# Kernel tuning notes

Hardware: AMD Instinct MI355X
Metric: run time of the kernel (lower is better)

## Reference

```python
import jax, jax.numpy as jnp
import numpy as np
import math

D_KEY = 64
D_VALUE = 64
NUM_HEADS = 16
D_MODEL = D_VALUE * NUM_HEADS  # 1024


def setup_inputs() -> dict:
    key = jax.random.key(0)
    ks = jax.random.split(key, 5)
    B, N = 2, 2048
    s = 1.0 / math.sqrt(D_MODEL)
    return {
        "x": jax.random.normal(ks[0], (B, N, D_MODEL), dtype=jnp.float32),
        "Wq": jax.random.normal(ks[1], (D_MODEL, D_KEY * NUM_HEADS), dtype=jnp.float32) * s,
        "Wk": jax.random.normal(ks[2], (D_MODEL, D_KEY * NUM_HEADS), dtype=jnp.float32) * s,
        "Wv": jax.random.normal(ks[3], (D_MODEL, D_MODEL), dtype=jnp.float32) * s,
        "Wp": jax.random.normal(ks[4], (D_MODEL, D_MODEL), dtype=jnp.float32) * s,
    }


def reference(x, Wq, Wk, Wv, Wp):
    # x: [B, N, d_model]. Equivalent to the original block-diagonal concat trick:
    # off-diagonal blocks are -inf, so softmax over the key axis reduces to
    # independent per-head softmax attention.
    B, N, D = x.shape
    H, K, V = NUM_HEADS, D_KEY, D_VALUE
    scale = 1.0 / math.sqrt(K)
    q = (x @ Wq).reshape(B, N, H, K)
    k = (x @ Wk).reshape(B, N, H, K)
    v = (x @ Wv).reshape(B, N, H, V)
    scores = jnp.einsum("bnhk,bmhk->bhnm", q, k) * scale  # [B,H,N,N]
    attn = jax.nn.softmax(scores, axis=-1)
    out = jnp.einsum("bhnm,bmhv->bnhv", attn, v).reshape(B, N, D)
    return x + out @ Wp
```

## Files before the change

kernel.cpp:

```cpp
#include <hip/hip_runtime.h>

typedef float f32x4 __attribute__((ext_vector_type(4)));
typedef __bf16 bf16x8 __attribute__((ext_vector_type(8)));

#define DEV static __device__ __forceinline__

DEV ushort f2bf(float f) {
  unsigned u = __builtin_bit_cast(unsigned, f);
  u += 0x7FFFu + ((u >> 16) & 1u);
  return (ushort)(u >> 16);
}

DEV bf16x8 ld_frag(const ushort* p) {
  return __builtin_bit_cast(bf16x8, *reinterpret_cast<const int4*>(p));
}

DEV bf16x8 ld_lds(const ushort* base, int byte_off) {
  return __builtin_bit_cast(bf16x8,
      *reinterpret_cast<const int4*>(reinterpret_cast<const char*>(base) + byte_off));
}

DEV int swz(int row, int col_byte) { return row * 128 + (col_byte ^ ((row & 7) << 4)); }

DEV float fast_exp2(float x) {
  float r;
  asm("v_exp_f32 %0, %1" : "=v"(r) : "v"(x));
  return r;
}

DEV unsigned cvt_pk_bf16(float lo, float hi) {
  unsigned r;
  asm("v_cvt_pk_bf16_f32 %0, %1, %2" : "=v"(r) : "v"(lo), "v"(hi));
  return r;
}

DEV void gload16(const ushort* g, ushort* l) {
  __builtin_amdgcn_global_load_lds(
      (const __attribute__((address_space(1))) unsigned int*)g,
      (__attribute__((address_space(3))) unsigned int*)l, 16, 0, 0);
}


__global__ __launch_bounds__(256) void convert_x(const float* __restrict__ x,
                                                 ushort* __restrict__ xb) {
  int i = blockIdx.x * 256 + threadIdx.x;
  float4 v = reinterpret_cast<const float4*>(x)[i];
  ushort4 o = make_ushort4(f2bf(v.x), f2bf(v.y), f2bf(v.z), f2bf(v.w));
  reinterpret_cast<ushort4*>(xb)[i] = o;
}

__global__ __launch_bounds__(256) void transpose_w(const float* __restrict__ w0,
                                                   const float* __restrict__ w1,
                                                   const float* __restrict__ w2,
                                                   const float* __restrict__ w3,
                                                   ushort* __restrict__ wt) {
  __shared__ float tile[32][33];
  const int z = blockIdx.z;
  const float* w = z == 0 ? w0 : z == 1 ? w1 : z == 2 ? w2 : w3;
  ushort* out = wt + (size_t)z * 1024 * 1024;
  const int n0 = blockIdx.x * 32, k0 = blockIdx.y * 32;
  const int tx = threadIdx.x, ty = threadIdx.y;
#pragma unroll
  for (int i = 0; i < 4; ++i)
    tile[ty + i * 8][tx] = w[(size_t)(k0 + ty + i * 8) * 1024 + n0 + tx];
  __syncthreads();
#pragma unroll
  for (int i = 0; i < 4; ++i)
    out[(size_t)(n0 + ty + i * 8) * 1024 + k0 + tx] = f2bf(tile[tx][ty + i * 8]);
}


DEV void gemm_core(const ushort* __restrict__ A, const ushort* __restrict__ BT,
                   ushort* a_lds, ushort* b_lds, int row0, int col0, f32x4 acc[4][4]) {
  const int tid = threadIdx.x;
  const int lane = tid & 63;
  const int w = tid >> 6, wr = w >> 1, wc = w & 1;
  const int lg = lane >> 4, l15 = lane & 15;
  const int srow = w * 32 + (lane >> 3);
  const int scol = ((lane & 7) ^ (lane >> 3)) << 3;
  const ushort* ga = A + (size_t)(row0 + srow) * 1024 + scol;
  const ushort* gb = BT + (size_t)(col0 + srow) * 1024 + scol;
#pragma unroll
  for (int ai = 0; ai < 4; ++ai)
#pragma unroll
    for (int bj = 0; bj < 4; ++bj) acc[ai][bj] = f32x4{0.f, 0.f, 0.f, 0.f};

  for (int kt = 0; kt < 1024; kt += 64) {
    __syncthreads();
#pragma unroll
    for (int p = 0; p < 4; ++p) {
      gload16(ga + kt + (size_t)(p * 8) * 1024, a_lds + (w * 32 + p * 8) * 64);
      gload16(gb + kt + (size_t)(p * 8) * 1024, b_lds + (w * 32 + p * 8) * 64);
    }
    __syncthreads();
    bf16x8 af[4][2], bfr[4][2];
#pragma unroll
    for (int i = 0; i < 4; ++i)
#pragma unroll
      for (int kk = 0; kk < 2; ++kk) {
        af[i][kk] = ld_lds(a_lds, swz(wr * 64 + i * 16 + l15, kk * 64 + lg * 16));
        bfr[i][kk] = ld_lds(b_lds, swz(wc * 64 + i * 16 + l15, kk * 64 + lg * 16));
      }
#pragma unroll
    for (int kk = 0; kk < 2; ++kk)
#pragma unroll
      for (int ai = 0; ai < 4; ++ai)
#pragma unroll
        for (int bj = 0; bj < 4; ++bj)
          acc[ai][bj] = __builtin_amdgcn_mfma_f32_16x16x32_bf16(af[ai][kk], bfr[bj][kk],
                                                                acc[ai][bj], 0, 0, 0);
  }
}

__global__ __launch_bounds__(256) void gemm_qkv(const ushort* __restrict__ xb,
                                                const ushort* __restrict__ wqT,
                                                const ushort* __restrict__ wkT,
                                                const ushort* __restrict__ wvT,
                                                ushort* __restrict__ q, ushort* __restrict__ k,
                                                ushort* __restrict__ vt) {
  __shared__ ushort a_lds[128 * 64], b_lds[128 * 64];
  const int fid = blockIdx.x;
  const int wid = (fid & 7) * 96 + (fid >> 3);
  const int row = wid / 24, rem = wid % 24;
  const int col = rem / 3, z = rem % 3;
  const int row0 = row * 128, col0 = col * 128;
  const ushort* BT = z == 0 ? wqT : z == 1 ? wkT : wvT;
  f32x4 acc[4][4];
  gemm_core(xb, BT, a_lds, b_lds, row0, col0, acc);
  const int lane = threadIdx.x & 63;
  const int w = threadIdx.x >> 6, wr = w >> 1, wc = w & 1;
  const int lg = lane >> 4, l15 = lane & 15;
  if (z < 2) {
    ushort* out = z == 0 ? q : k;
    const float sc = z == 0 ? 0.125f * 1.4426950408889634f : 1.0f;
#pragma unroll
    for (int ai = 0; ai < 4; ++ai)
#pragma unroll
      for (int bj = 0; bj < 4; ++bj)
#pragma unroll
        for (int r = 0; r < 4; ++r) {
          int orow = row0 + wr * 64 + ai * 16 + lg * 4 + r;
          int ocol = col0 + wc * 64 + bj * 16 + l15;
          out[(size_t)orow * 1024 + ocol] = f2bf(acc[ai][bj][r] * sc);
        }
  } else {
#pragma unroll
    for (int ai = 0; ai < 4; ++ai)
#pragma unroll
      for (int bj = 0; bj < 4; ++bj) {
        int orow = row0 + wr * 64 + ai * 16 + lg * 4;
        int ocol = col0 + wc * 64 + bj * 16 + l15;
        int bb = orow >> 11, n = orow & 2047;
        ushort4 pk = make_ushort4(f2bf(acc[ai][bj][0]), f2bf(acc[ai][bj][1]),
                                  f2bf(acc[ai][bj][2]), f2bf(acc[ai][bj][3]));
        *reinterpret_cast<ushort4*>(vt + ((size_t)(bb * 1024 + ocol)) * 2048 + n) = pk;
      }
  }
}

__global__ __launch_bounds__(256) void gemm_out(const ushort* __restrict__ ob,
                                                const ushort* __restrict__ wpT,
                                                const float* __restrict__ x,
                                                float* __restrict__ y) {
  __shared__ ushort a_lds[128 * 64], b_lds[64 * 64];
  const int fid = blockIdx.x;
  const int wid = (fid & 7) * 64 + (fid >> 3);
  const int row0 = (wid >> 4) * 128, col0 = (wid & 15) * 64;
  const int tid = threadIdx.x;
  const int lane = tid & 63;
  const int w = tid >> 6, wr = w >> 1, wc = w & 1;
  const int lg = lane >> 4, l15 = lane & 15;
  const int sr8 = lane >> 3;
  const int scol = ((lane & 7) ^ sr8) << 3;
  const ushort* ga = ob + (size_t)(row0 + w * 32 + sr8) * 1024 + scol;
  const ushort* gb = wpT + (size_t)(col0 + w * 16 + sr8) * 1024 + scol;

  f32x4 acc[4][2];
#pragma unroll
  for (int ai = 0; ai < 4; ++ai)
#pragma unroll
    for (int bj = 0; bj < 2; ++bj) acc[ai][bj] = f32x4{0.f, 0.f, 0.f, 0.f};

  for (int kt = 0; kt < 1024; kt += 64) {
    __syncthreads();
#pragma unroll
    for (int p = 0; p < 4; ++p)
      gload16(ga + kt + (size_t)(p * 8) * 1024, a_lds + (w * 32 + p * 8) * 64);
#pragma unroll
    for (int p = 0; p < 2; ++p)
      gload16(gb + kt + (size_t)(p * 8) * 1024, b_lds + (w * 16 + p * 8) * 64);
    __syncthreads();
    bf16x8 af[4][2], bfr[2][2];
#pragma unroll
    for (int kk = 0; kk < 2; ++kk) {
#pragma unroll
      for (int i = 0; i < 4; ++i)
        af[i][kk] = ld_lds(a_lds, swz(wr * 64 + i * 16 + l15, kk * 64 + lg * 16));
#pragma unroll
      for (int j = 0; j < 2; ++j)
        bfr[j][kk] = ld_lds(b_lds, swz(wc * 32 + j * 16 + l15, kk * 64 + lg * 16));
    }
#pragma unroll
    for (int kk = 0; kk < 2; ++kk)
#pragma unroll
      for (int ai = 0; ai < 4; ++ai)
#pragma unroll
        for (int bj = 0; bj < 2; ++bj)
          acc[ai][bj] = __builtin_amdgcn_mfma_f32_16x16x32_bf16(af[ai][kk], bfr[bj][kk],
                                                                acc[ai][bj], 0, 0, 0);
  }

#pragma unroll
  for (int ai = 0; ai < 4; ++ai)
#pragma unroll
    for (int bj = 0; bj < 2; ++bj)
#pragma unroll
      for (int r = 0; r < 4; ++r) {
        int orow = row0 + wr * 64 + ai * 16 + lg * 4 + r;
        int ocol = col0 + wc * 32 + bj * 16 + l15;
        size_t idx = (size_t)orow * 1024 + ocol;
        y[idx] = x[idx] + acc[ai][bj][r];
      }
}

__global__ __launch_bounds__(256) void attn(const ushort* __restrict__ qg,
                                            const ushort* __restrict__ kg,
                                            const ushort* __restrict__ vtg,
                                            ushort* __restrict__ og) {
  __shared__ ushort k_lds[4 * 64 * 64];
  __shared__ ushort v_lds[4 * 64 * 64];
  const int fid = blockIdx.x;
  const int wid = (fid & 7) * 64 + (fid >> 3);
  const int bh = wid >> 4, q0 = wid & 15;
  const int b = bh >> 4, h = bh & 15;
  const int n0 = q0 * 128;
  const int tid = threadIdx.x, lane = tid & 63, w = tid >> 6;
  const int lg = lane >> 4, l15 = lane & 15;

  bf16x8 qf[2][2];
#pragma unroll
  for (int qi = 0; qi < 2; ++qi)
#pragma unroll
    for (int d32 = 0; d32 < 2; ++d32)
      qf[qi][d32] = ld_frag(qg + (size_t)(b * 2048 + n0 + w * 32 + qi * 16 + l15) * 1024 +
                            h * 64 + d32 * 32 + lg * 8);

  f32x4 o[2][4];
#pragma unroll
  for (int qi = 0; qi < 2; ++qi)
#pragma unroll
    for (int bj = 0; bj < 4; ++bj) o[qi][bj] = f32x4{0.f, 0.f, 0.f, 0.f};
  f32x4 ssum[2] = {f32x4{0.f, 0.f, 0.f, 0.f}, f32x4{0.f, 0.f, 0.f, 0.f}};

  const int sr8 = lane >> 3;
  const int scol = ((lane & 7) ^ sr8) << 3;
  const ushort* kbase = kg + (size_t)(b * 2048 + w * 16 + sr8) * 1024 + h * 64 + scol;
  const ushort* vbase = vtg + (size_t)(b * 1024 + h * 64 + w * 16 + sr8) * 2048 + scol;

  auto stage_sub = [&](ushort* kdst, ushort* vdst, int kv0) {
#pragma unroll
    for (int p = 0; p < 2; ++p) {
      gload16(kbase + (size_t)(kv0 + p * 8) * 1024, kdst + (w * 16 + p * 8) * 64);
      gload16(vbase + (size_t)(p * 8) * 2048 + kv0, vdst + (w * 16 + p * 8) * 64);
    }
  };
  auto stage2 = [&](int buf, int kv0) {
    stage_sub(k_lds + (2 * buf) * 4096, v_lds + (2 * buf) * 4096, kv0);
    stage_sub(k_lds + (2 * buf + 1) * 4096, v_lds + (2 * buf + 1) * 4096, kv0 + 64);
  };

  const int4 ones4 = make_int4(0x3F803F80, 0x3F803F80, 0x3F803F80, 0x3F803F80);
  const bf16x8 onesf = __builtin_bit_cast(bf16x8, ones4);

  auto qk_sub = [&](const ushort* kb, f32x4 s[2][4]) {
#pragma unroll
    for (int qi = 0; qi < 2; ++qi)
#pragma unroll
      for (int kj = 0; kj < 4; ++kj) s[qi][kj] = f32x4{0.f, 0.f, 0.f, 0.f};
    __builtin_amdgcn_s_setprio(1);
#pragma unroll
    for (int d32 = 0; d32 < 2; ++d32)
#pragma unroll
      for (int kj = 0; kj < 4; ++kj) {
        bf16x8 kf = ld_lds(kb, swz(kj * 16 + l15, d32 * 64 + lg * 16));
        s[0][kj] = __builtin_amdgcn_mfma_f32_16x16x32_bf16(kf, qf[0][d32], s[0][kj], 0, 0, 0);
        s[1][kj] = __builtin_amdgcn_mfma_f32_16x16x32_bf16(kf, qf[1][d32], s[1][kj], 0, 0, 0);
      }
    __builtin_amdgcn_s_setprio(0);
  };

  auto sm_pv_sub = [&](const ushort* vb, f32x4 s[2][4]) {
    bf16x8 pa[2][2];
#pragma unroll
    for (int qi = 0; qi < 2; ++qi) {
      unsigned pk[4][2];
#pragma unroll
      for (int kj = 0; kj < 4; ++kj) {
        float p0 = fast_exp2(s[qi][kj][0]);
        float p1 = fast_exp2(s[qi][kj][1]);
        float p2 = fast_exp2(s[qi][kj][2]);
        float p3 = fast_exp2(s[qi][kj][3]);
        pk[kj][0] = cvt_pk_bf16(p0, p1);
        pk[kj][1] = cvt_pk_bf16(p2, p3);
      }
#pragma unroll
      for (int k32 = 0; k32 < 2; ++k32) {
        unsigned x0 = pk[2 * k32][0], y0 = pk[2 * k32 + 1][0];
        unsigned x1 = pk[2 * k32][1], y1 = pk[2 * k32 + 1][1];
        asm("v_permlane32_swap_b32 %0, %1" : "+v"(x0), "+v"(y0));
        asm("v_permlane32_swap_b32 %0, %1" : "+v"(x1), "+v"(y1));
        asm("v_permlane16_swap_b32 %0, %1" : "+v"(x0), "+v"(y0));
        asm("v_permlane16_swap_b32 %0, %1" : "+v"(x1), "+v"(y1));
        int4 fr = make_int4(x0, x1, y0, y1);
        pa[qi][k32] = __builtin_bit_cast(bf16x8, fr);
      }
    }
    __builtin_amdgcn_s_setprio(1);
#pragma unroll
    for (int qi = 0; qi < 2; ++qi) {
      ssum[qi] = __builtin_amdgcn_mfma_f32_16x16x32_bf16(pa[qi][0], onesf, ssum[qi], 0, 0, 0);
      ssum[qi] = __builtin_amdgcn_mfma_f32_16x16x32_bf16(pa[qi][1], onesf, ssum[qi], 0, 0, 0);
    }
#pragma unroll
    for (int k32 = 0; k32 < 2; ++k32)
#pragma unroll
      for (int bj = 0; bj < 4; ++bj) {
        bf16x8 vf = ld_lds(vb, swz(bj * 16 + l15, k32 * 64 + lg * 16));
        o[0][bj] = __builtin_amdgcn_mfma_f32_16x16x32_bf16(pa[0][k32], vf, o[0][bj], 0, 0, 0);
        o[1][bj] = __builtin_amdgcn_mfma_f32_16x16x32_bf16(pa[1][k32], vf, o[1][bj], 0, 0, 0);
      }
    __builtin_amdgcn_s_setprio(0);
  };

  auto body2 = [&](int buf) {
    const ushort* kb0 = k_lds + (2 * buf) * 4096;
    const ushort* kb1 = k_lds + (2 * buf + 1) * 4096;
    const ushort* vb0 = v_lds + (2 * buf) * 4096;
    const ushort* vb1 = v_lds + (2 * buf + 1) * 4096;
    f32x4 s0[2][4], s1[2][4];
    qk_sub(kb0, s0);
    qk_sub(kb1, s1);
    sm_pv_sub(vb0, s0);
    sm_pv_sub(vb1, s1);
  };

  stage2(0, 0);
  __syncthreads();

  for (int tt = 0; tt < 8; ++tt) {
    stage2(1, (2 * tt + 1) * 128);
    body2(0);
    __syncthreads();
    if (tt < 7) stage2(0, (2 * tt + 2) * 128);
    body2(1);
    __syncthreads();
  }

#pragma unroll
  for (int qi = 0; qi < 2; ++qi) {
    f32x4 inv;
#pragma unroll
    for (int r = 0; r < 4; ++r) inv[r] = 1.0f / ssum[qi][r];
#pragma unroll
    for (int bj = 0; bj < 4; ++bj)
#pragma unroll
      for (int r = 0; r < 4; ++r) {
        int n = n0 + w * 32 + qi * 16 + lg * 4 + r;
        og[(size_t)(b * 2048 + n) * 1024 + h * 64 + bj * 16 + l15] = f2bf(o[qi][bj][r] * inv[r]);
      }
  }
}


extern "C" void kernel_launch(void* const* d_in, const int* in_sizes, int n_in,
                              void* d_out, int out_size, void* d_ws, size_t ws_size,
                              hipStream_t stream) {
  const float* x = (const float*)d_in[0];
  const float* Wq = (const float*)d_in[1];
  const float* Wk = (const float*)d_in[2];
  const float* Wv = (const float*)d_in[3];
  const float* Wp = (const float*)d_in[4];
  float* y = (float*)d_out;

  char* ws = (char*)d_ws;
  ushort* xb = (ushort*)(ws);
  ushort* wT = (ushort*)(ws + (8ull << 20));
  ushort* qw = (ushort*)(ws + (16ull << 20));
  ushort* kw = (ushort*)(ws + (24ull << 20));
  ushort* vtw = (ushort*)(ws + (32ull << 20));
  ushort* ow = (ushort*)(ws);

  convert_x<<<4096, 256, 0, stream>>>(x, xb);
  transpose_w<<<dim3(32, 32, 4), dim3(32, 8), 0, stream>>>(Wq, Wk, Wv, Wp, wT);
  gemm_qkv<<<768, 256, 0, stream>>>(xb, wT, wT + (1u << 20), wT + (2u << 20), qw, kw, vtw);
  attn<<<512, 256, 0, stream>>>(qw, kw, vtw, ow);
  gemm_out<<<512, 256, 0, stream>>>(ow, wT + (3u << 20), x, y);
}
```

Measured before the change: 115.0 us.

## Split attention waves across KV halves with 64-row query tiles and LDS reduction

Each wave now handles 64 query rows but only half of every 64-key sub-tile (wave pairs split the KV dimension), rather than 32 query rows over all keys. Each K/V fragment read from LDS now feeds four MFMAs instead of two, which cuts LDS read traffic per MFMA. The partial O accumulators and row sums are combined at the end through an LDS reduction in which half the waves store and the other half add, normalize and write. The cost is higher register pressure (more Q fragments and accumulators), one extra barrier pair, and half the waves sitting idle during the final store.

Measured after the change: 132.6 us. 1.15x slower.

```diff
diff --git a/kernel.cpp b/kernel.cpp
--- a/kernel.cpp
+++ b/kernel.cpp
@@ -235,22 +235,24 @@
   const int b = bh >> 4, h = bh & 15;
   const int n0 = q0 * 128;
   const int tid = threadIdx.x, lane = tid & 63, w = tid >> 6;
+  const int wq = w >> 1, wkv = w & 1;
   const int lg = lane >> 4, l15 = lane & 15;
 
-  bf16x8 qf[2][2];
-#pragma unroll
-  for (int qi = 0; qi < 2; ++qi)
+  bf16x8 qf[4][2];
+#pragma unroll
+  for (int qi = 0; qi < 4; ++qi)
 #pragma unroll
     for (int d32 = 0; d32 < 2; ++d32)
-      qf[qi][d32] = ld_frag(qg + (size_t)(b * 2048 + n0 + w * 32 + qi * 16 + l15) * 1024 +
+      qf[qi][d32] = ld_frag(qg + (size_t)(b * 2048 + n0 + wq * 64 + qi * 16 + l15) * 1024 +
                             h * 64 + d32 * 32 + lg * 8);
 
-  f32x4 o[2][4];
-#pragma unroll
-  for (int qi = 0; qi < 2; ++qi)
+  f32x4 o[4][4];
+#pragma unroll
+  for (int qi = 0; qi < 4; ++qi)
 #pragma unroll
     for (int bj = 0; bj < 4; ++bj) o[qi][bj] = f32x4{0.f, 0.f, 0.f, 0.f};
-  f32x4 ssum[2] = {f32x4{0.f, 0.f, 0.f, 0.f}, f32x4{0.f, 0.f, 0.f, 0.f}};
+  f32x4 ssum[4] = {f32x4{0.f, 0.f, 0.f, 0.f}, f32x4{0.f, 0.f, 0.f, 0.f},
+                   f32x4{0.f, 0.f, 0.f, 0.f}, f32x4{0.f, 0.f, 0.f, 0.f}};
 
   const int sr8 = lane >> 3;
   const int scol = ((lane & 7) ^ sr8) << 3;
@@ -274,61 +276,56 @@
 
   auto qk_sub = [&](const ushort* kb, f32x4 s[2][4]) {
 #pragma unroll
-    for (int qi = 0; qi < 2; ++qi)
-#pragma unroll
-      for (int kj = 0; kj < 4; ++kj) s[qi][kj] = f32x4{0.f, 0.f, 0.f, 0.f};
+    for (int kj = 0; kj < 2; ++kj)
+#pragma unroll
+      for (int qi = 0; qi < 4; ++qi) s[kj][qi] = f32x4{0.f, 0.f, 0.f, 0.f};
     __builtin_amdgcn_s_setprio(1);
 #pragma unroll
     for (int d32 = 0; d32 < 2; ++d32)
 #pragma unroll
-      for (int kj = 0; kj < 4; ++kj) {
-        bf16x8 kf = ld_lds(kb, swz(kj * 16 + l15, d32 * 64 + lg * 16));
-        s[0][kj] = __builtin_amdgcn_mfma_f32_16x16x32_bf16(kf, qf[0][d32], s[0][kj], 0, 0, 0);
-        s[1][kj] = __builtin_amdgcn_mfma_f32_16x16x32_bf16(kf, qf[1][d32], s[1][kj], 0, 0, 0);
+      for (int kj = 0; kj < 2; ++kj) {
+        bf16x8 kf = ld_lds(kb, swz(wkv * 32 + kj * 16 + l15, d32 * 64 + lg * 16));
+#pragma unroll
+        for (int qi = 0; qi < 4; ++qi)
+          s[kj][qi] = __builtin_amdgcn_mfma_f32_16x16x32_bf16(kf, qf[qi][d32], s[kj][qi], 0, 0, 0);
       }
     __builtin_amdgcn_s_setprio(0);
   };
 
   auto sm_pv_sub = [&](const ushort* vb, f32x4 s[2][4]) {
-    bf16x8 pa[2][2];
-#pragma unroll
-    for (int qi = 0; qi < 2; ++qi) {
-      unsigned pk[4][2];
-#pragma unroll
-      for (int kj = 0; kj < 4; ++kj) {
-        float p0 = fast_exp2(s[qi][kj][0]);
-        float p1 = fast_exp2(s[qi][kj][1]);
-        float p2 = fast_exp2(s[qi][kj][2]);
-        float p3 = fast_exp2(s[qi][kj][3]);
+    bf16x8 pa[4];
+#pragma unroll
+    for (int qi = 0; qi < 4; ++qi) {
+      unsigned pk[2][2];
+#pragma unroll
+      for (int kj = 0; kj < 2; ++kj) {
+        float p0 = fast_exp2(s[kj][qi][0]);
+        float p1 = fast_exp2(s[kj][qi][1]);
+        float p2 = fast_exp2(s[kj][qi][2]);
+        float p3 = fast_exp2(s[kj][qi][3]);
         pk[kj][0] = cvt_pk_bf16(p0, p1);
         pk[kj][1] = cvt_pk_bf16(p2, p3);
       }
-#pragma unroll
-      for (int k32 = 0; k32 < 2; ++k32) {
-        unsigned x0 = pk[2 * k32][0], y0 = pk[2 * k32 + 1][0];
-        unsigned x1 = pk[2 * k32][1], y1 = pk[2 * k32 + 1][1];
-        asm("v_permlane32_swap_b32 %0, %1" : "+v"(x0), "+v"(y0));
-        asm("v_permlane32_swap_b32 %0, %1" : "+v"(x1), "+v"(y1));
-        asm("v_permlane16_swap_b32 %0, %1" : "+v"(x0), "+v"(y0));
-        asm("v_permlane16_swap_b32 %0, %1" : "+v"(x1), "+v"(y1));
-        int4 fr = make_int4(x0, x1, y0, y1);
-        pa[qi][k32] = __builtin_bit_cast(bf16x8, fr);
-      }
+      unsigned x0 = pk[0][0], y0 = pk[1][0];
+      unsigned x1 = pk[0][1], y1 = pk[1][1];
+      asm("v_permlane32_swap_b32 %0, %1" : "+v"(x0), "+v"(y0));
+      asm("v_permlane32_swap_b32 %0, %1" : "+v"(x1), "+v"(y1));
+      asm("v_permlane16_swap_b32 %0, %1" : "+v"(x0), "+v"(y0));
+      asm("v_permlane16_swap_b32 %0, %1" : "+v"(x1), "+v"(y1));
+      int4 fr = make_int4(x0, x1, y0, y1);
+      pa[qi] = __builtin_bit_cast(bf16x8, fr);
     }
     __builtin_amdgcn_s_setprio(1);
 #pragma unroll
-    for (int qi = 0; qi < 2; ++qi) {
-      ssum[qi] = __builtin_amdgcn_mfma_f32_16x16x32_bf16(pa[qi][0], onesf, ssum[qi], 0, 0, 0);
-      ssum[qi] = __builtin_amdgcn_mfma_f32_16x16x32_bf16(pa[qi][1], onesf, ssum[qi], 0, 0, 0);
-    }
-#pragma unroll
-    for (int k32 = 0; k32 < 2; ++k32)
-#pragma unroll
-      for (int bj = 0; bj < 4; ++bj) {
-        bf16x8 vf = ld_lds(vb, swz(bj * 16 + l15, k32 * 64 + lg * 16));
-        o[0][bj] = __builtin_amdgcn_mfma_f32_16x16x32_bf16(pa[0][k32], vf, o[0][bj], 0, 0, 0);
-        o[1][bj] = __builtin_amdgcn_mfma_f32_16x16x32_bf16(pa[1][k32], vf, o[1][bj], 0, 0, 0);
-      }
+    for (int qi = 0; qi < 4; ++qi)
+      ssum[qi] = __builtin_amdgcn_mfma_f32_16x16x32_bf16(pa[qi], onesf, ssum[qi], 0, 0, 0);
+#pragma unroll
+    for (int bj = 0; bj < 4; ++bj) {
+      bf16x8 vf = ld_lds(vb, swz(bj * 16 + l15, wkv * 64 + lg * 16));
+#pragma unroll
+      for (int qi = 0; qi < 4; ++qi)
+        o[qi][bj] = __builtin_amdgcn_mfma_f32_16x16x32_bf16(pa[qi], vf, o[qi][bj], 0, 0, 0);
+    }
     __builtin_amdgcn_s_setprio(0);
   };
 
@@ -356,18 +353,43 @@
     __syncthreads();
   }
 
-#pragma unroll
-  for (int qi = 0; qi < 2; ++qi) {
-    f32x4 inv;
-#pragma unroll
-    for (int r = 0; r < 4; ++r) inv[r] = 1.0f / ssum[qi][r];
-#pragma unroll
-    for (int bj = 0; bj < 4; ++bj)
-#pragma unroll
-      for (int r = 0; r < 4; ++r) {
-        int n = n0 + w * 32 + qi * 16 + lg * 4 + r;
-        og[(size_t)(b * 2048 + n) * 1024 + h * 64 + bj * 16 + l15] = f2bf(o[qi][bj][r] * inv[r]);
-      }
+  __syncthreads();
+  float* red = (float*)k_lds;
+  const int rbase = (wq * 64 + lane) * 84;
+  if (wkv == 1) {
+#pragma unroll
+    for (int qi = 0; qi < 4; ++qi)
+#pragma unroll
+      for (int bj = 0; bj < 4; ++bj)
+        *reinterpret_cast<f32x4*>(&red[rbase + (qi * 4 + bj) * 4]) = o[qi][bj];
+#pragma unroll
+    for (int qi = 0; qi < 4; ++qi)
+      *reinterpret_cast<f32x4*>(&red[rbase + 64 + qi * 4]) = ssum[qi];
+  }
+  __syncthreads();
+  if (wkv == 0) {
+#pragma unroll
+    for (int qi = 0; qi < 4; ++qi)
+#pragma unroll
+      for (int bj = 0; bj < 4; ++bj)
+        o[qi][bj] += *reinterpret_cast<const f32x4*>(&red[rbase + (qi * 4 + bj) * 4]);
+#pragma unroll
+    for (int qi = 0; qi < 4; ++qi)
+      ssum[qi] += *reinterpret_cast<const f32x4*>(&red[rbase + 64 + qi * 4]);
+#pragma unroll
+    for (int qi = 0; qi < 4; ++qi) {
+      f32x4 inv;
+#pragma unroll
+      for (int r = 0; r < 4; ++r) inv[r] = 1.0f / ssum[qi][r];
+#pragma unroll
+      for (int bj = 0; bj < 4; ++bj)
+#pragma unroll
+        for (int r = 0; r < 4; ++r) {
+          int n = n0 + wq * 64 + qi * 16 + lg * 4 + r;
+          og[(size_t)(b * 2048 + n) * 1024 + h * 64 + bj * 16 + l15] =
+              f2bf(o[qi][bj][r] * inv[r]);
+        }
+    }
   }
 }
 
```
